# Kernel tuning notes

Hardware: AMD Instinct MI355X
Metric: run time of the kernel (lower is better)

Reference implementation:

```python
import jax, jax.numpy as jnp
import numpy as np

DEGREES = [1, 2, 3]
SEG_IDS = np.repeat(np.arange(len(DEGREES)), [2 * l + 1 for l in DEGREES])  # (m_tot,)
M_TOT = int(SEG_IDS.shape[0])  # 15
N_NODES, F, F_IN, N_TYPE = 24576, 512, 512, 10


def setup_inputs() -> dict:
    key = jax.random.key(0)
    ks = jax.random.split(key, 8)
    s = 1.0 / np.sqrt(F).astype(np.float32)
    return {
        "x": jax.random.normal(ks[0], (N_NODES, F_IN), jnp.float32),
        "chi": jax.random.normal(ks[1], (N_NODES, M_TOT), jnp.float32),
        "z_one_hot": jax.nn.one_hot(jax.random.randint(ks[2], (N_NODES,), 0, N_TYPE), N_TYPE, dtype=jnp.float32),
        "W1": jax.random.normal(ks[3], (F_IN, F), jnp.float32) * s,
        "b1": jnp.zeros((F,), jnp.float32),
        "W2": jax.random.normal(ks[4], (F, F), jnp.float32) * s,
        "W3": jax.random.normal(ks[5], (F, 1), jnp.float32) * s,
        "W4": jax.random.normal(ks[6], (len(DEGREES) * F, F_IN), jnp.float32) * (1.0 / np.sqrt(len(DEGREES) * F).astype(np.float32)),
        "b4": jnp.zeros((F_IN,), jnp.float32),
    }


def _l0_contraction(x_chi):
    # make_l0_contraction_fn(degrees), vmapped over the feature axis:
    # per degree l, sum over its (2l+1) m-components of x_chi**2.
    # x_chi: (n, m_tot, F) -> (n, n_degrees, F)
    sq = jnp.swapaxes(x_chi * x_chi, 0, 1)  # (m_tot, n, F)
    out = jax.ops.segment_sum(sq, jnp.asarray(SEG_IDS), num_segments=len(DEGREES))
    return jnp.swapaxes(out, 0, 1)


def reference(x, chi, z_one_hot, W1, b1, W2, W3, W4, b4):
    # max_body_order == 2 -> SymmetricContraction branch is skipped (x_chi_bo = x_chi)
    h = x @ W1 + b1                              # Dense(features)(x): (n, F)
    x_chi = h[:, None, :] * chi[:, :, None]      # (n, m_tot, F)
    x_chi = x_chi @ W2                           # Dense(features, use_bias=False): (n, m_tot, F)
    chi_bo = (x_chi @ W3)[..., 0]                # Dense(1, use_bias=False).squeeze(-1): (n, m_tot)
    inv = _l0_contraction(x_chi).reshape(x.shape[0], -1)  # (n, n_degrees*F)
    x_bo = jax.nn.silu(inv @ W4 + b4)            # Dense(x.shape[-1]): (n, F_in)
    return (x_bo, chi_bo)
```

## Files before the change

### kernel.cpp

```cpp
#include <hip/hip_runtime.h>

typedef __bf16 bf16_t;
typedef __bf16 bf16x8 __attribute__((ext_vector_type(8)));
typedef __bf16 bf16x4 __attribute__((ext_vector_type(4)));
typedef float f32x4 __attribute__((ext_vector_type(4)));

#define BK 64
#define NNODES 24576


__device__ __forceinline__ void g2l16(const void* g, void* l) {
    __builtin_amdgcn_global_load_lds((__attribute__((address_space(1))) void*)(g),
                                     (__attribute__((address_space(3))) void*)(l),
                                     16, 0, 0);
}

#define SB()  __builtin_amdgcn_sched_barrier(0)
#define BAR() __builtin_amdgcn_s_barrier()

__global__ __launch_bounds__(1024)
void gemm16x_kernel(const float* __restrict__ X, const bf16_t* __restrict__ Bt,
                    const float* __restrict__ bias, bf16_t* __restrict__ A3,
                    const float* __restrict__ W3, const float* __restrict__ c3v,
                    float* __restrict__ sbuf)
{
    __shared__ __align__(16) char smem[114688];
    char* baseA = smem;
    char* baseB = smem + 49152;

    const int tid  = threadIdx.x;
    const int lane = tid & 63;
    const int wave = tid >> 6;
    const int wr   = wave >> 2;
    const int wc   = wave & 3;
    const int l15  = lane & 15;
    const int lh   = lane >> 4;

    const int bm = blockIdx.x;
    const int bn = blockIdx.y;

    const size_t strbB = 1024;

    const int q0 = tid * 16;
    const size_t roB = (size_t)(q0 >> 7) * strbB + ((q0 ^ (((q0 >> 7) & 7) << 4)) & 127);
    const char* gB = (const char*)Bt + (size_t)bn * 256 * strbB + roB;

    auto stageB = [&](int t, int buf) {
        const size_t kb = (size_t)t * 128;
        g2l16(gB + kb,                baseB + buf * 32768 + q0);
        g2l16(gB + kb + 128 * strbB,  baseB + buf * 32768 + 16384 + q0);
    };

    const int arow0 = tid >> 4;
    const int e4    = (tid & 15) * 4;
    const float* gx = X + (size_t)(bm * 192 + arow0) * 512 + e4;
    const int woff0 = ((arow0 * 128) + e4 * 2) ^ ((arow0 & 7) << 4);

    float4 fA[3];
    auto loadA = [&](int t) {
#pragma unroll
        for (int r = 0; r < 3; ++r)
            fA[r] = *(const float4*)(gx + (size_t)r * 64 * 512 + t * 64);
    };
    auto writeA = [&](int buf) {
        char* d = baseA + buf * 24576;
#pragma unroll
        for (int r = 0; r < 3; ++r) {
            bf16x4 o;
            o[0] = (bf16_t)fA[r].x; o[1] = (bf16_t)fA[r].y;
            o[2] = (bf16_t)fA[r].z; o[3] = (bf16_t)fA[r].w;
            *(bf16x4*)(d + r * 8192 + woff0) = o;
        }
    };

    const int swzr = (l15 & 7) << 4;
    const int xk0  = (lh * 16) ^ swzr;
    const int xk1  = (64 + lh * 16) ^ swzr;
    const int aOff = (wr * 48 + l15) * 128;
    const int bOff = (wc * 64 + l15) * 128;

    f32x4 acc[3][4] = {};

    loadA(0); stageB(0, 0);
    asm volatile("s_waitcnt vmcnt(2)" ::: "memory");
    writeA(0);

    for (int t = 0; t < 8; ++t) {
        const int buf = t & 1;

        asm volatile("s_waitcnt vmcnt(0) lgkmcnt(0)" ::: "memory");
        BAR();
        SB();

        if (t < 7) { loadA(t + 1); stageB(t + 1, buf ^ 1); }
        SB();

        bf16x8 af[3][2], bf[4][2];
        {
            const char* _pa = baseA + buf * 24576 + aOff;
#pragma unroll
            for (int m = 0; m < 3; ++m) {
                af[m][0] = *(const bf16x8*)(_pa + m * 2048 + xk0);
                af[m][1] = *(const bf16x8*)(_pa + m * 2048 + xk1);
            }
            const char* _pb = baseB + buf * 32768 + bOff;
#pragma unroll
            for (int n = 0; n < 4; ++n) {
                bf[n][0] = *(const bf16x8*)(_pb + n * 2048 + xk0);
                bf[n][1] = *(const bf16x8*)(_pb + n * 2048 + xk1);
            }
        }

        __builtin_amdgcn_s_setprio(1);
#pragma unroll
        for (int m = 0; m < 3; ++m)
#pragma unroll
        for (int n = 0; n < 4; ++n)
#pragma unroll
        for (int kk = 0; kk < 2; ++kk)
            acc[m][n] = __builtin_amdgcn_mfma_f32_16x16x32_bf16(
                af[m][kk], bf[n][kk], acc[m][n], 0, 0, 0);
        __builtin_amdgcn_s_setprio(0);

        if (t < 7) {
            asm volatile("s_waitcnt vmcnt(2)" ::: "memory");
            SB();
            writeA(buf ^ 1);
        }
        SB();
    }

    BAR();
    bf16_t* sg = (bf16_t*)smem;
    const int gr0 = bm * 192 + wr * 48 + lh * 4;
    const int gc0 = bn * 256 + wc * 64 + l15;
    const int lr0 = wr * 48 + lh * 4;
    const int lc0 = wc * 64 + l15;
    float w3v[4], bv[4];
#pragma unroll
    for (int n = 0; n < 4; ++n) {
        w3v[n] = W3[gc0 + n * 16];
        bv[n]  = bias[gc0 + n * 16];
    }
#pragma unroll
    for (int m = 0; m < 3; ++m)
#pragma unroll
    for (int j = 0; j < 4; ++j) {
        const int r = gr0 + m * 16 + j;
        float g[4], p = 0.f;
#pragma unroll
        for (int n = 0; n < 4; ++n) {
            g[n] = acc[m][n][j] + bv[n];
            p += g[n] * w3v[n];
        }
        p += __shfl_xor(p, 1); p += __shfl_xor(p, 2);
        p += __shfl_xor(p, 4); p += __shfl_xor(p, 8);
        if (l15 == 0) atomicAdd(&sbuf[r], p);
        bf16_t* srow = sg + (lr0 + m * 16 + j) * 264 + lc0;
#pragma unroll
        for (int n = 0; n < 4; ++n)
            srow[n * 16] = (bf16_t)(g[n] * g[n]);
    }
    BAR();
    const int rl = tid >> 5;
    const int cb = (tid & 31) * 8;
#pragma unroll
    for (int pass = 0; pass < 6; ++pass) {
        const int row = pass * 32 + rl;
        const bf16x8 v = *(const bf16x8*)((const char*)sg + row * 528 + cb * 2);
        float f[8];
#pragma unroll
        for (int j = 0; j < 8; ++j) f[j] = (float)v[j];
        const int grow = bm * 192 + row;
#pragma unroll
        for (int l = 0; l < 3; ++l) {
            const float c = c3v[grow + l * NNODES];
            bf16x8 o;
#pragma unroll
            for (int j = 0; j < 8; ++j) o[j] = (bf16_t)(c * f[j]);
            *(bf16x8*)(A3 + (size_t)grow * 1536 + l * 512 + bn * 256 + cb) = o;
        }
    }
}

__global__ __launch_bounds__(1024)
void gemm16_kernel(const bf16_t* __restrict__ A, const bf16_t* __restrict__ Bt,
                   const float* __restrict__ bias, void* __restrict__ Cout,
                   int N, int K, int mode)
{
    __shared__ __align__(16) bf16_t lA[2][12288];
    __shared__ __align__(16) bf16_t lB[2][16384];

    const int tid  = threadIdx.x;
    const int lane = tid & 63;
    const int wave = tid >> 6;
    const int wr   = wave >> 2;
    const int wc   = wave & 3;
    const int l15  = lane & 15;
    const int lh   = lane >> 4;

    const int bm = blockIdx.x;
    const int bn = blockIdx.y;

    const size_t strb = (size_t)K * 2;

    const int q0 = tid * 16;
    const size_t ro = (size_t)(q0 >> 7) * strb + ((q0 ^ (((q0 >> 7) & 7) << 4)) & 127);
    const char* gA = (const char*)A  + (size_t)bm * 192 * strb + ro;
    const char* gB = (const char*)Bt + (size_t)bn * 256 * strb + ro;
    char* baseA = (char*)&lA[0][0];
    char* baseB = (char*)&lB[0][0];

    auto stage = [&](int t, int buf) {
        const size_t kb = (size_t)t * 128;
        g2l16(gA + kb, baseA + buf * 24576 + q0);
        if (tid < 512)
            g2l16(gA + kb + 128 * strb, baseA + buf * 24576 + 16384 + q0);
        g2l16(gB + kb, baseB + buf * 32768 + q0);
        g2l16(gB + kb + 128 * strb, baseB + buf * 32768 + 16384 + q0);
    };

    const int swzr = (l15 & 7) << 4;
    const int xk0  = (lh * 16) ^ swzr;
    const int xk1  = (64 + lh * 16) ^ swzr;
    const int aOff = (wr * 48 + l15) * 128;
    const int bOff = (wc * 64 + l15) * 128;

    f32x4 acc[3][4] = {};

    const int T = K / BK;
    stage(0, 0);

    for (int t = 0; t < T; ++t) {
        const int buf = t & 1;

        asm volatile("s_waitcnt vmcnt(0)" ::: "memory");
        BAR();
        SB();

        if (t + 1 < T) stage(t + 1, buf ^ 1);
        SB();

        bf16x8 af[3][2], bf[4][2];
        {
            const char* _pa = baseA + buf * 24576 + aOff;
#pragma unroll
            for (int m = 0; m < 3; ++m) {
                af[m][0] = *(const bf16x8*)(_pa + m * 2048 + xk0);
                af[m][1] = *(const bf16x8*)(_pa + m * 2048 + xk1);
            }
            const char* _pb = baseB + buf * 32768 + bOff;
#pragma unroll
            for (int n = 0; n < 4; ++n) {
                bf[n][0] = *(const bf16x8*)(_pb + n * 2048 + xk0);
                bf[n][1] = *(const bf16x8*)(_pb + n * 2048 + xk1);
            }
        }

        __builtin_amdgcn_s_setprio(1);
#pragma unroll
        for (int m = 0; m < 3; ++m)
#pragma unroll
        for (int n = 0; n < 4; ++n)
#pragma unroll
        for (int kk = 0; kk < 2; ++kk)
            acc[m][n] = __builtin_amdgcn_mfma_f32_16x16x32_bf16(
                af[m][kk], bf[n][kk], acc[m][n], 0, 0, 0);
        __builtin_amdgcn_s_setprio(0);
    }

    const int gr0 = bm * 192 + wr * 48 + lh * 4;
    const int gc0 = bn * 256 + wc * 64 + l15;
    if (mode == 0) {
        bf16_t* C = (bf16_t*)Cout;
#pragma unroll
        for (int m = 0; m < 3; ++m)
#pragma unroll
        for (int n = 0; n < 4; ++n) {
            const int c = gc0 + n * 16;
            const float bv = bias ? bias[c] : 0.f;
#pragma unroll
            for (int j = 0; j < 4; ++j)
                C[(size_t)(gr0 + m * 16 + j) * N + c] = (bf16_t)(acc[m][n][j] + bv);
        }
    } else {
        float* C = (float*)Cout;
#pragma unroll
        for (int m = 0; m < 3; ++m)
#pragma unroll
        for (int n = 0; n < 4; ++n) {
            const int c = gc0 + n * 16;
            const float bv = bias[c];
#pragma unroll
            for (int j = 0; j < 4; ++j) {
                float v = acc[m][n][j] + bv;
                C[(size_t)(gr0 + m * 16 + j) * N + c] = v / (1.f + __expf(-v));
            }
        }
    }
}

__global__ __launch_bounds__(512)
void gemm8_kernel(const bf16_t* __restrict__ A, const bf16_t* __restrict__ Bt,
                  void* __restrict__ Cout, int N, int K, int LD)
{
    __shared__ __align__(16) bf16_t lA[2][16384];
    __shared__ __align__(16) bf16_t lB[2][16384];

    const int tid  = threadIdx.x;
    const int lane = tid & 63;
    const int wave = tid >> 6;
    const int wr   = wave >> 2;
    const int wc   = wave & 3;
    const int l15  = lane & 15;
    const int lh   = lane >> 4;

    const int bm = blockIdx.x;
    const int bn = blockIdx.y;
    const int bz = blockIdx.z;

    const size_t strb = (size_t)LD * 2;
    const size_t zoff = (size_t)bz * K * 2;

    const int q0 = tid * 16;
    const size_t rowOff = (size_t)(q0 >> 7) * strb + ((q0 ^ (((q0 >> 7) & 7) << 4)) & 127);
    const char* gA = (const char*)A  + (size_t)bm * 256 * strb + zoff + rowOff;
    const char* gB = (const char*)Bt + (size_t)bn * 256 * strb + zoff + rowOff;
    char* baseA = (char*)&lA[0][0];
    char* baseB = (char*)&lB[0][0];

    auto stageA = [&](int t, int buf, int r) {
        g2l16(gA + (size_t)t * 128 + (size_t)(r * 64) * strb,
              baseA + buf * 32768 + r * 8192 + q0);
    };
    auto stageB = [&](int t, int buf, int r) {
        g2l16(gB + (size_t)t * 128 + (size_t)(r * 64) * strb,
              baseB + buf * 32768 + r * 8192 + q0);
    };

    const int swzr = (l15 & 7) << 4;
    const int xk0  = (lh * 16) ^ swzr;
    const int xk1  = (64 + lh * 16) ^ swzr;
    const int aOff = wr * 16384 + l15 * 128;
    const int bOff = wc * 8192 + l15 * 128;

    f32x4 acc[2][2][4][2] = {};

    const int T = K / BK;

#pragma unroll
    for (int r = 0; r < 4; ++r) { stageA(0, 0, r); stageB(0, 0, r); }

    for (int t = 0; t < T; ++t) {
        const int buf = t & 1, nbuf = buf ^ 1;

        asm volatile("s_waitcnt vmcnt(0)" ::: "memory");
        BAR();
        SB();

        if (t + 1 < T) {
#pragma unroll
            for (int r = 0; r < 4; ++r) { stageA(t + 1, nbuf, r); stageB(t + 1, nbuf, r); }
        }
        SB();

        bf16x8 af[8][2], bf[4][2];
        {
            const char* _pa = baseA + buf * 32768 + aOff;
#pragma unroll
            for (int i = 0; i < 8; ++i) {
                af[i][0] = *(const bf16x8*)(_pa + i * 2048 + xk0);
                af[i][1] = *(const bf16x8*)(_pa + i * 2048 + xk1);
            }
            const char* _pb = baseB + buf * 32768 + bOff;
#pragma unroll
            for (int j = 0; j < 4; ++j) {
                bf[j][0] = *(const bf16x8*)(_pb + j * 2048 + xk0);
                bf[j][1] = *(const bf16x8*)(_pb + j * 2048 + xk1);
            }
        }

        __builtin_amdgcn_s_setprio(1);
#pragma unroll
        for (int mh = 0; mh < 2; ++mh)
#pragma unroll
        for (int nh = 0; nh < 2; ++nh)
#pragma unroll
        for (int m = 0; m < 4; ++m)
#pragma unroll
        for (int n = 0; n < 2; ++n)
#pragma unroll
        for (int kk = 0; kk < 2; ++kk)
            acc[mh][nh][m][n] = __builtin_amdgcn_mfma_f32_16x16x32_bf16(
                af[mh * 4 + m][kk], bf[nh * 2 + n][kk], acc[mh][nh][m][n], 0, 0, 0);
        __builtin_amdgcn_s_setprio(0);
    }

    float* C = (float*)Cout + (size_t)bz * 512 * 512;
    const int gr0 = bm * 256 + wr * 128 + lh * 4;
    const int gc0 = bn * 256 + wc * 64 + l15;
#pragma unroll
    for (int mh = 0; mh < 2; ++mh)
#pragma unroll
    for (int nh = 0; nh < 2; ++nh)
#pragma unroll
    for (int m = 0; m < 4; ++m)
#pragma unroll
    for (int n = 0; n < 2; ++n) {
        const int c = gc0 + nh * 32 + n * 16;
#pragma unroll
        for (int j = 0; j < 4; ++j)
            C[(size_t)(gr0 + (mh * 4 + m) * 16 + j) * N + c] = acc[mh][nh][m][n][j];
    }
}

__global__ void wct_reduce_kernel(const float* __restrict__ p, bf16_t* __restrict__ out) {
    const int i = blockIdx.x * 256 + threadIdx.x;
    out[i] = (bf16_t)(p[i] + p[i + 262144] + p[i + 524288] + p[i + 786432]);
}

__global__ void prepw1_kernel(const float* __restrict__ W1, bf16_t* __restrict__ W1b) {
    const int i = blockIdx.x * 256 + threadIdx.x;
    const float4* p = (const float4*)W1 + (size_t)i * 2;
    float4 a = p[0], c = p[1];
    bf16x8 v;
    v[0] = (bf16_t)a.x; v[1] = (bf16_t)a.y; v[2] = (bf16_t)a.z; v[3] = (bf16_t)a.w;
    v[4] = (bf16_t)c.x; v[5] = (bf16_t)c.y; v[6] = (bf16_t)c.z; v[7] = (bf16_t)c.w;
    *(bf16x8*)(W1b + (size_t)i * 8) = v;
}

__global__ __launch_bounds__(256)
void tr_kernel(const float* __restrict__ in, bf16_t* __restrict__ out, int R, int C) {
    __shared__ float tile[64][65];
    const int c0 = blockIdx.x * 64, r0 = blockIdx.y * 64;
    const int tx = threadIdx.x & 63, ty = threadIdx.x >> 6;
#pragma unroll
    for (int p = 0; p < 16; ++p) {
        const int r = p * 4 + ty;
        tile[r][tx] = in[(size_t)(r0 + r) * C + c0 + tx];
    }
    __syncthreads();
#pragma unroll
    for (int p = 0; p < 16; ++p) {
        const int c = p * 4 + ty;
        out[(size_t)(c0 + c) * R + r0 + tx] = (bf16_t)tile[tx][c];
    }
}

__global__ void vecmat_kernel(const float* __restrict__ v, const float* __restrict__ W,
                              float* __restrict__ out) {
    const int t = blockIdx.x * blockDim.x + threadIdx.x;
    if (t >= 512) return;
    float s = 0.f;
    for (int i = 0; i < 512; ++i) s += v[i] * W[i * 512 + t];
    out[t] = s;
}

__global__ void c3_kernel(const float* __restrict__ chi, float* __restrict__ c3,
                          float* __restrict__ sbuf) {
    const int n = blockIdx.x * 256 + threadIdx.x;
    if (n >= NNODES) return;
    const float* ch = chi + (size_t)n * 15;
    float a = 0.f, b = 0.f, c = 0.f;
#pragma unroll
    for (int m = 0; m < 3; ++m)  a += ch[m] * ch[m];
#pragma unroll
    for (int m = 3; m < 8; ++m)  b += ch[m] * ch[m];
#pragma unroll
    for (int m = 8; m < 15; ++m) c += ch[m] * ch[m];
    c3[n] = a; c3[n + NNODES] = b; c3[n + 2 * NNODES] = c;
    sbuf[n] = 0.f;
}

__global__ void chbo_kernel(const float* __restrict__ chi, const float* __restrict__ s,
                            float* __restrict__ chbo) {
    const int idx = blockIdx.x * 256 + threadIdx.x;
    if (idx >= NNODES * 15) return;
    chbo[idx] = chi[idx] * s[idx / 15];
}

extern "C" void kernel_launch(void* const* d_in, const int* in_sizes, int n_in,
                              void* d_out, int out_size, void* d_ws, size_t ws_size,
                              hipStream_t stream)
{
    const float* x   = (const float*)d_in[0];
    const float* chi = (const float*)d_in[1];
    const float* W1  = (const float*)d_in[3];
    const float* b1  = (const float*)d_in[4];
    const float* W2  = (const float*)d_in[5];
    const float* W3  = (const float*)d_in[6];
    const float* W4  = (const float*)d_in[7];
    const float* b4  = (const float*)d_in[8];

    char* ws = (char*)d_ws;
    bf16_t* W1b  = (bf16_t*)(ws + 0);
    bf16_t* W4t  = (bf16_t*)(ws + 1048576);
    bf16_t* Wct  = (bf16_t*)(ws + 2621440);
    float*  bc   = (float*) (ws + 3145728);
    bf16_t* W2t  = (bf16_t*)(ws + 3147776);
    bf16_t* A3   = (bf16_t*)(ws + 3674112);
    float*  Wctp = (float*) (ws + 3674112);

    float*  xbo  = (float*)d_out;
    float*  chbo = (float*)d_out + (size_t)NNODES * 512;
    char*   c0s  = (char*)d_out;
    float*  c3   = (float*) (c0s + 25165824);
    float*  sbuf = (float*) (c0s + 25460736);

    prepw1_kernel<<<128, 256, 0, stream>>>(W1, W1b);
    tr_kernel<<<dim3(8, 8),  256, 0, stream>>>(W2, W2t, 512, 512);
    tr_kernel<<<dim3(8, 24), 256, 0, stream>>>(W4, W4t, 1536, 512);
    vecmat_kernel<<<2, 256, 0, stream>>>(b1, W2, bc);
    c3_kernel<<<96, 256, 0, stream>>>(chi, c3, sbuf);

    gemm8_kernel<<<dim3(2, 2, 4), 512, 0, stream>>>(W2t, W1b, Wctp, 512, 128, 512);
    wct_reduce_kernel<<<1024, 256, 0, stream>>>(Wctp, Wct);

    gemm16x_kernel<<<dim3(128, 2), 1024, 0, stream>>>(x, Wct, bc, A3, W3, c3, sbuf);

    chbo_kernel<<<1440, 256, 0, stream>>>(chi, sbuf, chbo);

    gemm16_kernel<<<dim3(128, 2), 1024, 0, stream>>>(A3, W4t, b4, xbo, 512, 1536, 1);
}
```

Baseline: 139.5 us.

## Apply per-degree chi scaling inside final GEMM instead of materializing A3

```diff
diff --git a/kernel.cpp b/kernel.cpp
--- a/kernel.cpp
+++ b/kernel.cpp
@@ -18,11 +18,17 @@
 #define SB()  __builtin_amdgcn_sched_barrier(0)
 #define BAR() __builtin_amdgcn_s_barrier()
 
+__device__ __forceinline__ bf16x8 scale8(bf16x8 v, float c) {
+    bf16x8 o;
+#pragma unroll
+    for (int j = 0; j < 8; ++j) o[j] = (bf16_t)(c * (float)v[j]);
+    return o;
+}
+
 __global__ __launch_bounds__(1024)
 void gemm16x_kernel(const float* __restrict__ X, const bf16_t* __restrict__ Bt,
-                    const float* __restrict__ bias, bf16_t* __restrict__ A3,
-                    const float* __restrict__ W3, const float* __restrict__ c3v,
-                    float* __restrict__ sbuf)
+                    const float* __restrict__ bias, bf16_t* __restrict__ G2,
+                    const float* __restrict__ W3, float* __restrict__ sbuf)
 {
     __shared__ __align__(16) char smem[114688];
     char* baseA = smem;
@@ -168,28 +174,18 @@
     for (int pass = 0; pass < 6; ++pass) {
         const int row = pass * 32 + rl;
         const bf16x8 v = *(const bf16x8*)((const char*)sg + row * 528 + cb * 2);
-        float f[8];
-#pragma unroll
-        for (int j = 0; j < 8; ++j) f[j] = (float)v[j];
-        const int grow = bm * 192 + row;
-#pragma unroll
-        for (int l = 0; l < 3; ++l) {
-            const float c = c3v[grow + l * NNODES];
-            bf16x8 o;
-#pragma unroll
-            for (int j = 0; j < 8; ++j) o[j] = (bf16_t)(c * f[j]);
-            *(bf16x8*)(A3 + (size_t)grow * 1536 + l * 512 + bn * 256 + cb) = o;
-        }
+        *(bf16x8*)(G2 + (size_t)(bm * 192 + row) * 512 + bn * 256 + cb) = v;
     }
 }
 
 __global__ __launch_bounds__(1024)
-void gemm16_kernel(const bf16_t* __restrict__ A, const bf16_t* __restrict__ Bt,
-                   const float* __restrict__ bias, void* __restrict__ Cout,
-                   int N, int K, int mode)
+void gemm16g_kernel(const bf16_t* __restrict__ G2, const bf16_t* __restrict__ W4t,
+                    const float* __restrict__ b4, const float* __restrict__ c3v,
+                    float* __restrict__ xbo)
 {
-    __shared__ __align__(16) bf16_t lA[2][12288];
-    __shared__ __align__(16) bf16_t lB[2][16384];
+    __shared__ __align__(16) char smem[147456];
+    char* baseA = smem;
+    char* baseB = smem + 49152;
 
     const int tid  = threadIdx.x;
     const int lane = tid & 63;
@@ -202,46 +198,49 @@
     const int bm = blockIdx.x;
     const int bn = blockIdx.y;
 
-    const size_t strb = (size_t)K * 2;
-
     const int q0 = tid * 16;
-    const size_t ro = (size_t)(q0 >> 7) * strb + ((q0 ^ (((q0 >> 7) & 7) << 4)) & 127);
-    const char* gA = (const char*)A  + (size_t)bm * 192 * strb + ro;
-    const char* gB = (const char*)Bt + (size_t)bn * 256 * strb + ro;
-    char* baseA = (char*)&lA[0][0];
-    char* baseB = (char*)&lB[0][0];
+    const int swc = (q0 ^ (((q0 >> 7) & 7) << 4)) & 127;
+    const char* gA = (const char*)G2 + ((size_t)(bm * 192) + (q0 >> 7)) * 1024 + swc;
+    const char* gB = (const char*)W4t + ((size_t)(bn * 128) + (q0 >> 7)) * 3072 + swc;
 
     auto stage = [&](int t, int buf) {
         const size_t kb = (size_t)t * 128;
         g2l16(gA + kb, baseA + buf * 24576 + q0);
         if (tid < 512)
-            g2l16(gA + kb + 128 * strb, baseA + buf * 24576 + 16384 + q0);
-        g2l16(gB + kb, baseB + buf * 32768 + q0);
-        g2l16(gB + kb + 128 * strb, baseB + buf * 32768 + 16384 + q0);
+            g2l16(gA + kb + (size_t)128 * 1024, baseA + buf * 24576 + 16384 + q0);
+#pragma unroll
+        for (int l = 0; l < 3; ++l)
+            g2l16(gB + kb + l * 1024, baseB + buf * 49152 + l * 16384 + q0);
     };
 
     const int swzr = (l15 & 7) << 4;
     const int xk0  = (lh * 16) ^ swzr;
     const int xk1  = (64 + lh * 16) ^ swzr;
     const int aOff = (wr * 48 + l15) * 128;
-    const int bOff = (wc * 64 + l15) * 128;
-
-    f32x4 acc[3][4] = {};
-
-    const int T = K / BK;
+    const int bOff = (wc * 32 + l15) * 128;
+
+    float cv[3][3];
+#pragma unroll
+    for (int l = 0; l < 3; ++l)
+#pragma unroll
+        for (int m = 0; m < 3; ++m)
+            cv[l][m] = c3v[l * NNODES + bm * 192 + wr * 48 + m * 16 + l15];
+
+    f32x4 acc[3][2] = {};
+
     stage(0, 0);
 
-    for (int t = 0; t < T; ++t) {
+    for (int t = 0; t < 8; ++t) {
         const int buf = t & 1;
 
         asm volatile("s_waitcnt vmcnt(0)" ::: "memory");
         BAR();
         SB();
 
-        if (t + 1 < T) stage(t + 1, buf ^ 1);
-        SB();
-
-        bf16x8 af[3][2], bf[4][2];
+        if (t < 7) stage(t + 1, buf ^ 1);
+        SB();
+
+        bf16x8 af[3][2];
         {
             const char* _pa = baseA + buf * 24576 + aOff;
 #pragma unroll
@@ -249,53 +248,46 @@
                 af[m][0] = *(const bf16x8*)(_pa + m * 2048 + xk0);
                 af[m][1] = *(const bf16x8*)(_pa + m * 2048 + xk1);
             }
-            const char* _pb = baseB + buf * 32768 + bOff;
-#pragma unroll
-            for (int n = 0; n < 4; ++n) {
-                bf[n][0] = *(const bf16x8*)(_pb + n * 2048 + xk0);
-                bf[n][1] = *(const bf16x8*)(_pb + n * 2048 + xk1);
-            }
-        }
-
-        __builtin_amdgcn_s_setprio(1);
-#pragma unroll
-        for (int m = 0; m < 3; ++m)
-#pragma unroll
-        for (int n = 0; n < 4; ++n)
-#pragma unroll
-        for (int kk = 0; kk < 2; ++kk)
-            acc[m][n] = __builtin_amdgcn_mfma_f32_16x16x32_bf16(
-                af[m][kk], bf[n][kk], acc[m][n], 0, 0, 0);
-        __builtin_amdgcn_s_setprio(0);
+        }
+
+#pragma unroll
+        for (int l = 0; l < 3; ++l) {
+            bf16x8 bfr[2][2];
+            const char* _pb = baseB + buf * 49152 + l * 16384 + bOff;
+#pragma unroll
+            for (int n = 0; n < 2; ++n) {
+                bfr[n][0] = *(const bf16x8*)(_pb + n * 2048 + xk0);
+                bfr[n][1] = *(const bf16x8*)(_pb + n * 2048 + xk1);
+            }
+            __builtin_amdgcn_s_setprio(1);
+#pragma unroll
+            for (int m = 0; m < 3; ++m) {
+                const bf16x8 as0 = scale8(af[m][0], cv[l][m]);
+                const bf16x8 as1 = scale8(af[m][1], cv[l][m]);
+#pragma unroll
+                for (int n = 0; n < 2; ++n) {
+                    acc[m][n] = __builtin_amdgcn_mfma_f32_16x16x32_bf16(
+                        as0, bfr[n][0], acc[m][n], 0, 0, 0);
+                    acc[m][n] = __builtin_amdgcn_mfma_f32_16x16x32_bf16(
+                        as1, bfr[n][1], acc[m][n], 0, 0, 0);
+                }
+            }
+            __builtin_amdgcn_s_setprio(0);
+        }
     }
 
     const int gr0 = bm * 192 + wr * 48 + lh * 4;
-    const int gc0 = bn * 256 + wc * 64 + l15;
-    if (mode == 0) {
-        bf16_t* C = (bf16_t*)Cout;
-#pragma unroll
-        for (int m = 0; m < 3; ++m)
-#pragma unroll
-        for (int n = 0; n < 4; ++n) {
-            const int c = gc0 + n * 16;
-            const float bv = bias ? bias[c] : 0.f;
-#pragma unroll
-            for (int j = 0; j < 4; ++j)
-                C[(size_t)(gr0 + m * 16 + j) * N + c] = (bf16_t)(acc[m][n][j] + bv);
-        }
-    } else {
-        float* C = (float*)Cout;
-#pragma unroll
-        for (int m = 0; m < 3; ++m)
-#pragma unroll
-        for (int n = 0; n < 4; ++n) {
-            const int c = gc0 + n * 16;
-            const float bv = bias[c];
-#pragma unroll
-            for (int j = 0; j < 4; ++j) {
-                float v = acc[m][n][j] + bv;
-                C[(size_t)(gr0 + m * 16 + j) * N + c] = v / (1.f + __expf(-v));
-            }
+    const int gc0 = bn * 128 + wc * 32 + l15;
+#pragma unroll
+    for (int m = 0; m < 3; ++m)
+#pragma unroll
+    for (int n = 0; n < 2; ++n) {
+        const int c = gc0 + n * 16;
+        const float bv = b4[c];
+#pragma unroll
+        for (int j = 0; j < 4; ++j) {
+            float v = acc[m][n][j] + bv;
+            xbo[(size_t)(gr0 + m * 16 + j) * 512 + c] = v / (1.f + __expf(-v));
         }
     }
 }
@@ -494,18 +486,17 @@
 
     char* ws = (char*)d_ws;
     bf16_t* W1b  = (bf16_t*)(ws + 0);
+    float*  c3   = (float*) (ws + 524288);
+    float*  sbuf = (float*) (ws + 819200);
     bf16_t* W4t  = (bf16_t*)(ws + 1048576);
     bf16_t* Wct  = (bf16_t*)(ws + 2621440);
     float*  bc   = (float*) (ws + 3145728);
     bf16_t* W2t  = (bf16_t*)(ws + 3147776);
-    bf16_t* A3   = (bf16_t*)(ws + 3674112);
+    bf16_t* G2   = (bf16_t*)(ws + 3674112);
     float*  Wctp = (float*) (ws + 3674112);
 
     float*  xbo  = (float*)d_out;
     float*  chbo = (float*)d_out + (size_t)NNODES * 512;
-    char*   c0s  = (char*)d_out;
-    float*  c3   = (float*) (c0s + 25165824);
-    float*  sbuf = (float*) (c0s + 25460736);
 
     prepw1_kernel<<<128, 256, 0, stream>>>(W1, W1b);
     tr_kernel<<<dim3(8, 8),  256, 0, stream>>>(W2, W2t, 512, 512);
@@ -516,9 +507,9 @@
     gemm8_kernel<<<dim3(2, 2, 4), 512, 0, stream>>>(W2t, W1b, Wctp, 512, 128, 512);
     wct_reduce_kernel<<<1024, 256, 0, stream>>>(Wctp, Wct);
 
-    gemm16x_kernel<<<dim3(128, 2), 1024, 0, stream>>>(x, Wct, bc, A3, W3, c3, sbuf);
+    gemm16x_kernel<<<dim3(128, 2), 1024, 0, stream>>>(x, Wct, bc, G2, W3, sbuf);
 
     chbo_kernel<<<1440, 256, 0, stream>>>(chi, sbuf, chbo);
 
-    gemm16_kernel<<<dim3(128, 2), 1024, 0, stream>>>(A3, W4t, b4, xbo, 512, 1536, 1);
-}
+    gemm16g_kernel<<<dim3(128, 4), 1024, 0, stream>>>(G2, W4t, b4, c3, xbo);
+}
```

Measured after the change: 173.8 us. 1.25x slower.
